# Kernel tuning notes

Hardware: AMD Instinct MI355X
Metric: run time of the kernel (lower is better)

The kernel has to match this reference:

```python
import jax, jax.numpy as jnp
import numpy as np

N_NODES = 50000
N_EDGES = 500000
F_IN = 128
HIDDEN = 128
N_CLASSES = 32
N_GRAPHS = 64


def setup_inputs() -> dict:
    key = jax.random.key(0)
    ks = jax.random.split(key, 16)
    x = jax.random.normal(ks[0], (N_NODES, F_IN), dtype=jnp.float32)
    edge_index = jax.random.randint(ks[1], (2, N_EDGES), 0, N_NODES, dtype=jnp.int64)
    batch = jnp.sort(jax.random.randint(ks[2], (N_NODES,), 0, N_GRAPHS, dtype=jnp.int64))
    d = {"x": x, "edge_index": edge_index, "batch": batch}
    dims = [(F_IN, HIDDEN)] + [(HIDDEN, HIDDEN)] * 4
    for i, (fi, fo) in enumerate(dims, start=1):
        s = 1.0 / np.sqrt(fi)
        d[f"W{i}"] = jax.random.uniform(ks[2 + i], (fi, fo), jnp.float32, -s, s)
        d[f"b{i}"] = jnp.zeros((fo,), jnp.float32)
    s = 1.0 / np.sqrt(HIDDEN)
    d["W_lin"] = jax.random.uniform(ks[10], (HIDDEN, N_CLASSES), jnp.float32, -s, s)
    d["b_lin"] = jnp.zeros((N_CLASSES,), jnp.float32)
    return d


def _gcn_conv(x, W, b, src, dst, norm_edge, norm_self):
    # PyG GCNConv: h = x @ W; out[dst] += norm * h[src]; + self-loop + bias
    h = x @ W
    msg = h[src] * norm_edge[:, None]                      # [E, F] gather + scale
    agg = jax.ops.segment_sum(msg, dst, num_segments=x.shape[0])  # scatter-add
    return agg + h * norm_self[:, None] + b


def reference(x, edge_index, batch, W1, b1, W2, b2, W3, b3, W4, b4, W5, b5, W_lin, b_lin):
    src, dst = edge_index[0], edge_index[1]
    n = x.shape[0]
    # degree with self-loops (in-degree at dst, +1 for the self loop)
    deg = jax.ops.segment_sum(jnp.ones_like(dst, dtype=x.dtype), dst, num_segments=n) + 1.0
    dis = jax.lax.rsqrt(deg)
    norm_edge = dis[src] * dis[dst]   # per-edge symmetric normalization
    norm_self = dis * dis             # self-loop coefficient = 1/deg

    h = jax.nn.relu(_gcn_conv(x, W1, b1, src, dst, norm_edge, norm_self))
    h = jax.nn.relu(_gcn_conv(h, W2, b2, src, dst, norm_edge, norm_self))
    h = jax.nn.relu(_gcn_conv(h, W3, b3, src, dst, norm_edge, norm_self))
    h = jax.nn.relu(_gcn_conv(h, W4, b4, src, dst, norm_edge, norm_self))
    h = _gcn_conv(h, W5, b5, src, dst, norm_edge, norm_self)

    # global mean pool over graphs in the batch
    sums = jax.ops.segment_sum(h, batch, num_segments=N_GRAPHS)
    counts = jax.ops.segment_sum(jnp.ones((n,), h.dtype), batch, num_segments=N_GRAPHS)
    pooled = sums / jnp.maximum(counts, 1.0)[:, None]
    # dropout is identity in eval mode
    return pooled @ W_lin + b_lin
```

## Files before the change

kernel.cpp:

```cpp
#include <hip/hip_runtime.h>
#include <hip/hip_bf16.h>

#define N_NODES   50000
#define N_EDGES   500000
#define FDIM      128
#define N_CLASSES 32
#define N_GRAPHS  64


__global__ void deg_kernel(const int* __restrict__ dst, int* __restrict__ deg, int E) {
    int e = blockIdx.x * blockDim.x + threadIdx.x;
    if (e < E) atomicAdd(&deg[dst[e]], 1);
}

__global__ void scan_partial(const int* __restrict__ deg, int* __restrict__ part,
                             float* __restrict__ dis, int n) {
    __shared__ int s[512];
    int t = threadIdx.x;
    int i = blockIdx.x * 512 + t;
    int d = (i < n) ? deg[i] : 0;
    if (i < n) dis[i] = rsqrtf((float)d + 1.0f);
    s[t] = (i < n) ? ((d + 3) & ~3) : 0;
    __syncthreads();
    for (int o = 256; o > 0; o >>= 1) {
        if (t < o) s[t] += s[t + o];
        __syncthreads();
    }
    if (t == 0) part[blockIdx.x] = s[0];
}

__global__ void scan_offsets(int* part, int nb) {
    if (blockIdx.x == 0 && threadIdx.x == 0) {
        int acc = 0;
        for (int i = 0; i < nb; i++) { int v = part[i]; part[i] = acc; acc += v; }
    }
}

__global__ void scan_final(const int* __restrict__ deg, const int* __restrict__ part,
                           int* __restrict__ rowptr, int n) {
    __shared__ int s[512];
    int t = threadIdx.x;
    int i = blockIdx.x * 512 + t;
    int v = (i < n) ? ((deg[i] + 3) & ~3) : 0;
    s[t] = v;
    __syncthreads();
    for (int o = 1; o < 512; o <<= 1) {
        int x = (t >= o) ? s[t - o] : 0;
        __syncthreads();
        s[t] += x;
        __syncthreads();
    }
    if (i < n) rowptr[i] = part[blockIdx.x] + s[t] - v;
}

__global__ void fill_csr(const int* __restrict__ src, const int* __restrict__ dst,
                         const int* __restrict__ rowptr, int* __restrict__ fill,
                         const float* __restrict__ dis,
                         int2* __restrict__ csr_sw, int E) {
    int e = blockIdx.x * blockDim.x + threadIdx.x;
    if (e >= E) return;
    int d = dst[e], s = src[e];
    int pos = rowptr[d] + atomicAdd(&fill[d], 1);
    float w = dis[s] * dis[d];
    csr_sw[pos] = make_int2(s, __float_as_int(w));
}

__global__ void pad_csr(const int* __restrict__ deg, const int* __restrict__ rowptr,
                        int2* __restrict__ csr_sw, int n) {
    int v = blockIdx.x * blockDim.x + threadIdx.x;
    if (v >= n) return;
    int d = deg[v], dp = (d + 3) & ~3;
    int base = rowptr[v];
    for (int i = d; i < dp; i++) csr_sw[base + i] = make_int2(v, 0);
}


#define PGATH(I, EBASE)                                                         \
    int2 p##I = sw[(EBASE) + 2 * (I) + half];                                   \
    float4 m##I = *(const float4*)(H + (size_t)p##I.x * FDIM + q * 4);

#define PFMA(I)                                                                 \
    {                                                                           \
        float w_ = __int_as_float(p##I.y);                                      \
        acc.x = fmaf(w_, m##I.x, acc.x);                                        \
        acc.y = fmaf(w_, m##I.y, acc.y);                                        \
        acc.z = fmaf(w_, m##I.z, acc.z);                                        \
        acc.w = fmaf(w_, m##I.w, acc.w);                                        \
    }

__global__ __launch_bounds__(256) void fused_layer(const float* __restrict__ H,
                                                   const float* __restrict__ W,
                                                   const float* __restrict__ bias,
                                                   float* __restrict__ OUT,
                                                   const int* __restrict__ rowptr,
                                                   const int* __restrict__ degi,
                                                   const int2* __restrict__ csr_sw,
                                                   const float* __restrict__ dis,
                                                   int n, int relu) {
    __shared__ __align__(16) float xs[FDIM][36];
    __shared__ __align__(16) float ws[32][132];
    int t = threadIdx.x;
    int lane = t & 63;
    int wv = t >> 6;
    int half = lane >> 5;
    int q = lane & 31;
    int rowBase = blockIdx.x * 32;

    for (int i = 0; i < 8; i++) {
        int r = wv * 8 + i;
        int v = rowBase + r;
        float4 acc = make_float4(0.f, 0.f, 0.f, 0.f);
        if (v < n) {
            const int2* sw = csr_sw + rowptr[v];
            int cnt = (degi[v] + 3) & ~3;
            int e = 0;
            for (; e + 16 <= cnt; e += 16) {
                PGATH(0, e) PGATH(1, e) PGATH(2, e) PGATH(3, e)
                PGATH(4, e) PGATH(5, e) PGATH(6, e) PGATH(7, e)
                PFMA(0) PFMA(1) PFMA(2) PFMA(3) PFMA(4) PFMA(5) PFMA(6) PFMA(7)
            }
            if (e + 8 <= cnt) {
                PGATH(0, e) PGATH(1, e) PGATH(2, e) PGATH(3, e)
                PFMA(0) PFMA(1) PFMA(2) PFMA(3)
                e += 8;
            }
            if (e + 4 <= cnt) {
                PGATH(0, e) PGATH(1, e)
                PFMA(0) PFMA(1)
            }
            acc.x += __shfl_xor(acc.x, 32);
            acc.y += __shfl_xor(acc.y, 32);
            acc.z += __shfl_xor(acc.z, 32);
            acc.w += __shfl_xor(acc.w, 32);
            float dv = dis[v];
            float ns = dv * dv;
            float4 hv = *(const float4*)(H + (size_t)v * FDIM + q * 4);
            acc.x = fmaf(ns, hv.x, acc.x);
            acc.y = fmaf(ns, hv.y, acc.y);
            acc.z = fmaf(ns, hv.z, acc.z);
            acc.w = fmaf(ns, hv.w, acc.w);
        }
        if (half == 0) {
            xs[q * 4 + 0][r] = acc.x;
            xs[q * 4 + 1][r] = acc.y;
            xs[q * 4 + 2][r] = acc.z;
            xs[q * 4 + 3][r] = acc.w;
        }
    }

    int ti = t & 7;
    int tj = t >> 3;
    float acc2[4][4];
#pragma unroll
    for (int r = 0; r < 4; r++)
#pragma unroll
        for (int c = 0; c < 4; c++) acc2[r][c] = 0.f;

    for (int k0 = 0; k0 < 128; k0 += 32) {
        __syncthreads();
        {
            int c4 = t & 31, kr = t >> 5;
#pragma unroll
            for (int p = 0; p < 4; p++) {
                int k = kr + 8 * p;
                float4 v = *(const float4*)(W + (size_t)(k0 + k) * FDIM + c4 * 4);
                *(float4*)&ws[k][c4 * 4] = v;
            }
        }
        __syncthreads();
#pragma unroll 8
        for (int k = 0; k < 32; k++) {
            float4 a = *(const float4*)&xs[k0 + k][ti * 4];
            float4 b = *(const float4*)&ws[k][tj * 4];
            float ar[4] = {a.x, a.y, a.z, a.w};
            float br[4] = {b.x, b.y, b.z, b.w};
#pragma unroll
            for (int r = 0; r < 4; r++)
#pragma unroll
                for (int c = 0; c < 4; c++) acc2[r][c] = fmaf(ar[r], br[c], acc2[r][c]);
        }
    }

    float4 bb = *(const float4*)(bias + tj * 4);
#pragma unroll
    for (int rr = 0; rr < 4; rr++) {
        int grow = rowBase + ti * 4 + rr;
        if (grow < n) {
            float4 o;
            o.x = acc2[rr][0] + bb.x;
            o.y = acc2[rr][1] + bb.y;
            o.z = acc2[rr][2] + bb.z;
            o.w = acc2[rr][3] + bb.w;
            if (relu) {
                o.x = fmaxf(o.x, 0.f); o.y = fmaxf(o.y, 0.f);
                o.z = fmaxf(o.z, 0.f); o.w = fmaxf(o.w, 0.f);
            }
            *(float4*)(OUT + (size_t)grow * FDIM + tj * 4) = o;
        }
    }
}


#define POOL_BLOCKS 1024

__global__ __launch_bounds__(128) void pool_kernel(const float* __restrict__ H,
                                                   const int* __restrict__ batch,
                                                   float* __restrict__ psum,
                                                   float* __restrict__ pcnt, int n) {
    int t = threadIdx.x;
    int chunk = (n + POOL_BLOCKS - 1) / POOL_BLOCKS;
    int lo = blockIdx.x * chunk;
    int hi = lo + chunk; if (hi > n) hi = n;
    if (lo >= hi) return;

    float acc = 0.f;
    int cnt = 0;
    int curg = batch[lo];
    float hv = H[(size_t)lo * FDIM + t];
    int g = curg;
    for (int v = lo; v < hi; v++) {
        float hcur = hv;
        int gcur = g;
        if (v + 1 < hi) {
            hv = H[(size_t)(v + 1) * FDIM + t];
            g = batch[v + 1];
        }
        if (gcur != curg) {
            atomicAdd(&psum[curg * FDIM + t], acc);
            if (t == 0) atomicAdd(&pcnt[curg], (float)cnt);
            acc = 0.f; cnt = 0; curg = gcur;
        }
        acc += hcur;
        cnt++;
    }
    atomicAdd(&psum[curg * FDIM + t], acc);
    if (t == 0) atomicAdd(&pcnt[curg], (float)cnt);
}

__global__ void final_lin(const float* __restrict__ psum, const float* __restrict__ pcnt,
                          const float* __restrict__ Wl, const float* __restrict__ bl,
                          float* __restrict__ out) {
    int t = blockIdx.x * blockDim.x + threadIdx.x;
    if (t >= N_GRAPHS * N_CLASSES) return;
    int g = t >> 5, c = t & 31;
    float inv = 1.0f / fmaxf(pcnt[g], 1.0f);
    float s = 0.f;
    for (int k = 0; k < FDIM; k++) s = fmaf(psum[g * FDIM + k], Wl[k * N_CLASSES + c], s);
    out[t] = s * inv + bl[c];
}


static inline size_t align256(size_t x) { return (x + 255) & ~(size_t)255; }

extern "C" void kernel_launch(void* const* d_in, const int* in_sizes, int n_in,
                              void* d_out, int out_size, void* d_ws, size_t ws_size,
                              hipStream_t stream) {
    const float* x     = (const float*)d_in[0];
    const int*   ei    = (const int*)d_in[1];
    const int*   batch = (const int*)d_in[2];
    const float* Wls[5] = {(const float*)d_in[3], (const float*)d_in[5], (const float*)d_in[7],
                           (const float*)d_in[9], (const float*)d_in[11]};
    const float* bls[5] = {(const float*)d_in[4], (const float*)d_in[6], (const float*)d_in[8],
                           (const float*)d_in[10], (const float*)d_in[12]};
    const float* W_lin = (const float*)d_in[13];
    const float* b_lin = (const float*)d_in[14];
    float* out = (float*)d_out;

    const int N = N_NODES, E = N_EDGES;
    const int* src = ei;
    const int* dst = ei + E;

    char* p = (char*)d_ws;
    size_t off = 0;
    float* hA = (float*)(p + off); off = align256(off + (size_t)N * FDIM * 4);
    float* hB = (float*)(p + off); off = align256(off + (size_t)N * FDIM * 4);
    int2*  csr_sw = (int2*)(p + off); off = align256(off + ((size_t)E + 4 * N) * 8);
    float* dis = (float*)(p + off); off = align256(off + (size_t)N * 4);
    int*   rowptr = (int*)(p + off); off = align256(off + (size_t)N * 4);
    int*   part = (int*)(p + off); off = align256(off + 512);
    size_t zero_off = off;
    int*   deg = (int*)(p + off); off = align256(off + (size_t)N * 4);
    int*   fill = (int*)(p + off); off = align256(off + (size_t)N * 4);
    float* psum = (float*)(p + off); off = align256(off + (size_t)N_GRAPHS * FDIM * 4);
    float* pcnt = (float*)(p + off); off = align256(off + (size_t)N_GRAPHS * 4);
    size_t zero_bytes = off - zero_off;
    (void)ws_size; (void)n_in; (void)in_sizes; (void)out_size;

    hipMemsetAsync(p + zero_off, 0, zero_bytes, stream);

    deg_kernel<<<(E + 255) / 256, 256, 0, stream>>>(dst, deg, E);
    int nChunks = (N + 511) / 512;
    scan_partial<<<nChunks, 512, 0, stream>>>(deg, part, dis, N);
    scan_offsets<<<1, 64, 0, stream>>>(part, nChunks);
    scan_final<<<nChunks, 512, 0, stream>>>(deg, part, rowptr, N);
    fill_csr<<<(E + 255) / 256, 256, 0, stream>>>(src, dst, rowptr, fill, dis,
                                                  csr_sw, E);
    pad_csr<<<(N + 255) / 256, 256, 0, stream>>>(deg, rowptr, csr_sw, N);

    int fusedBlocks = (N + 31) / 32;
    const float* cur = x;
    float* bufs[2] = {hA, hB};
    for (int l = 0; l < 5; l++) {
        float* dst_h = bufs[l & 1];
        int relu = (l < 4) ? 1 : 0;
        fused_layer<<<fusedBlocks, 256, 0, stream>>>(cur, Wls[l], bls[l], dst_h,
                                                     rowptr, deg, csr_sw, dis, N, relu);
        cur = dst_h;
    }

    pool_kernel<<<POOL_BLOCKS, 128, 0, stream>>>(hA, batch, psum, pcnt, N);
    final_lin<<<(N_GRAPHS * N_CLASSES + 255) / 256, 256, 0, stream>>>(psum, pcnt, W_lin,
                                                                      b_lin, out);
}
```

Before: 419.7 us.

## Read W directly from global memory and XOR-swizzle aggregated tile in LDS

The fused GCN layer no longer stages W through shared memory in four chunks. Each thread now reads its float4 of W straight from global or L2 memory in the GEMM loop. The aggregated 32-row tile is stored in a padding-free XOR-swizzled layout to avoid bank conflicts. This removes the ws buffer and its per-chunk barriers, which cuts LDS use and may raise occupancy. In exchange the loop issues many global loads of W and replaces vector LDS reads with four scalar ones.

```diff
diff --git a/kernel.cpp b/kernel.cpp
--- a/kernel.cpp
+++ b/kernel.cpp
@@ -97,8 +97,7 @@
                                                    const int2* __restrict__ csr_sw,
                                                    const float* __restrict__ dis,
                                                    int n, int relu) {
-    __shared__ __align__(16) float xs[FDIM][36];
-    __shared__ __align__(16) float ws[32][132];
+    __shared__ float xs[FDIM * 32];
     int t = threadIdx.x;
     int lane = t & 63;
     int wv = t >> 6;
@@ -141,12 +140,14 @@
             acc.w = fmaf(ns, hv.w, acc.w);
         }
         if (half == 0) {
-            xs[q * 4 + 0][r] = acc.x;
-            xs[q * 4 + 1][r] = acc.y;
-            xs[q * 4 + 2][r] = acc.z;
-            xs[q * 4 + 3][r] = acc.w;
-        }
-    }
+            int col = r ^ q;
+            xs[(q * 4 + 0) * 32 + col] = acc.x;
+            xs[(q * 4 + 1) * 32 + col] = acc.y;
+            xs[(q * 4 + 2) * 32 + col] = acc.z;
+            xs[(q * 4 + 3) * 32 + col] = acc.w;
+        }
+    }
+    __syncthreads();
 
     int ti = t & 7;
     int tj = t >> 3;
@@ -156,29 +157,31 @@
 #pragma unroll
         for (int c = 0; c < 4; c++) acc2[r][c] = 0.f;
 
-    for (int k0 = 0; k0 < 128; k0 += 32) {
-        __syncthreads();
-        {
-            int c4 = t & 31, kr = t >> 5;
-#pragma unroll
-            for (int p = 0; p < 4; p++) {
-                int k = kr + 8 * p;
-                float4 v = *(const float4*)(W + (size_t)(k0 + k) * FDIM + c4 * 4);
-                *(float4*)&ws[k][c4 * 4] = v;
-            }
-        }
-        __syncthreads();
-#pragma unroll 8
-        for (int k = 0; k < 32; k++) {
-            float4 a = *(const float4*)&xs[k0 + k][ti * 4];
-            float4 b = *(const float4*)&ws[k][tj * 4];
-            float ar[4] = {a.x, a.y, a.z, a.w};
-            float br[4] = {b.x, b.y, b.z, b.w};
-#pragma unroll
-            for (int r = 0; r < 4; r++)
-#pragma unroll
-                for (int c = 0; c < 4; c++) acc2[r][c] = fmaf(ar[r], br[c], acc2[r][c]);
-        }
+#pragma unroll 4
+    for (int k = 0; k < 128; k++) {
+        float4 b = *(const float4*)(W + (size_t)k * FDIM + tj * 4);
+        int swz = k >> 2;
+        int base = k * 32;
+        float a0 = xs[base + ((ti * 4 + 0) ^ swz)];
+        float a1 = xs[base + ((ti * 4 + 1) ^ swz)];
+        float a2 = xs[base + ((ti * 4 + 2) ^ swz)];
+        float a3 = xs[base + ((ti * 4 + 3) ^ swz)];
+        acc2[0][0] = fmaf(a0, b.x, acc2[0][0]);
+        acc2[0][1] = fmaf(a0, b.y, acc2[0][1]);
+        acc2[0][2] = fmaf(a0, b.z, acc2[0][2]);
+        acc2[0][3] = fmaf(a0, b.w, acc2[0][3]);
+        acc2[1][0] = fmaf(a1, b.x, acc2[1][0]);
+        acc2[1][1] = fmaf(a1, b.y, acc2[1][1]);
+        acc2[1][2] = fmaf(a1, b.z, acc2[1][2]);
+        acc2[1][3] = fmaf(a1, b.w, acc2[1][3]);
+        acc2[2][0] = fmaf(a2, b.x, acc2[2][0]);
+        acc2[2][1] = fmaf(a2, b.y, acc2[2][1]);
+        acc2[2][2] = fmaf(a2, b.z, acc2[2][2]);
+        acc2[2][3] = fmaf(a2, b.w, acc2[2][3]);
+        acc2[3][0] = fmaf(a3, b.x, acc2[3][0]);
+        acc2[3][1] = fmaf(a3, b.y, acc2[3][1]);
+        acc2[3][2] = fmaf(a3, b.z, acc2[3][2]);
+        acc2[3][3] = fmaf(a3, b.w, acc2[3][3]);
     }
 
     float4 bb = *(const float4*)(bias + tj * 4);
```

Result: slower. 481.4 us (+14.7%).
